# Optimization experiments

Hardware: AMD Instinct MI355X
Metric: run time of the kernel (lower is better)

## Reference

```python
import jax, jax.numpy as jnp
import numpy as np

B, S, H = 2, 2048, 2048
NUM_HEADS, NUM_KV_HEADS, HEAD_DIM = 8, 1, 256
ROPE_THETA = 10000.0
NEG_INF = -1e9


def _rope_tables(seq_len, head_dim, base=ROPE_THETA):
    # cos/sin of shape [seq_len, head_dim], matching GemmaRotaryEmbedding
    inv_freq = 1.0 / (base ** (jnp.arange(0, head_dim, 2, dtype=jnp.float32) / head_dim))
    pos = jnp.arange(seq_len, dtype=jnp.float32)
    freqs = pos[:, None] * inv_freq[None, :]          # [S, D/2]
    emb = jnp.concatenate([freqs, freqs], axis=-1)    # [S, D]
    return jnp.cos(emb), jnp.sin(emb)


def _rotate_half(x):
    d = x.shape[-1] // 2
    return jnp.concatenate([-x[..., d:], x[..., :d]], axis=-1)


def setup_inputs() -> dict:
    key = jax.random.key(0)
    ks = jax.random.split(key, 5)
    hidden_states = jax.random.normal(ks[0], (B, S, H), dtype=jnp.float32)
    # additive causal mask: 0 where allowed, -inf above diagonal
    causal = jnp.tril(jnp.ones((S, S), dtype=bool))
    attention_mask = jnp.where(causal, 0.0, NEG_INF).astype(jnp.float32)[None, None]  # [1,1,S,S]
    sc = 1.0 / np.sqrt(H)
    Wq = jax.random.normal(ks[1], (H, NUM_HEADS * HEAD_DIM), dtype=jnp.float32) * sc
    Wk = jax.random.normal(ks[2], (H, NUM_KV_HEADS * HEAD_DIM), dtype=jnp.float32) * sc
    Wv = jax.random.normal(ks[3], (H, NUM_KV_HEADS * HEAD_DIM), dtype=jnp.float32) * sc
    Wo = jax.random.normal(ks[4], (NUM_HEADS * HEAD_DIM, H), dtype=jnp.float32) * sc
    return {"hidden_states": hidden_states, "attention_mask": attention_mask,
            "Wq": Wq, "Wk": Wk, "Wv": Wv, "Wo": Wo}


def reference(hidden_states, attention_mask, Wq, Wk, Wv, Wo):
    b, s, _ = hidden_states.shape
    g = NUM_HEADS // NUM_KV_HEADS  # query heads per kv head

    q = (hidden_states @ Wq).reshape(b, s, NUM_HEADS, HEAD_DIM).transpose(0, 2, 1, 3)      # [b,h,s,d]
    k = (hidden_states @ Wk).reshape(b, s, NUM_KV_HEADS, HEAD_DIM).transpose(0, 2, 1, 3)   # [b,kh,s,d]
    v = (hidden_states @ Wv).reshape(b, s, NUM_KV_HEADS, HEAD_DIM).transpose(0, 2, 1, 3)   # [b,kh,s,d]

    cos, sin = _rope_tables(s, HEAD_DIM)  # [s,d]
    cos = cos[None, None]                 # [1,1,s,d]
    sin = sin[None, None]
    q = q * cos + _rotate_half(q) * sin
    k = k * cos + _rotate_half(k) * sin

    # GQA attention without materializing repeated K/V: group query heads per kv head
    qg = q.reshape(b, NUM_KV_HEADS, g, s, HEAD_DIM)                       # [b,kh,g,s,d]
    scale = 1.0 / np.sqrt(HEAD_DIM)
    scores = jnp.einsum('bkgsd,bktd->bkgst', qg, k) * scale               # [b,kh,g,s,t]
    scores = scores + attention_mask[:, :, None]                          # broadcast [1,1,1,s,t]
    probs = jax.nn.softmax(scores, axis=-1)
    out = jnp.einsum('bkgst,bktd->bkgsd', probs, v)                       # [b,kh,g,s,d]
    out = out.reshape(b, NUM_HEADS, s, HEAD_DIM).transpose(0, 2, 1, 3).reshape(b, s, NUM_HEADS * HEAD_DIM)
    return out @ Wo
```

## Files before the change

### kernel.cpp

```cpp
#include <hip/hip_runtime.h>

typedef unsigned short u16;
typedef short short8 __attribute__((ext_vector_type(8)));
typedef float f32x4 __attribute__((ext_vector_type(4)));
typedef float f32x16 __attribute__((ext_vector_type(16)));
typedef u16 u16x4 __attribute__((ext_vector_type(4)));

__device__ __forceinline__ u16 f2bf(float f) {
    unsigned int u = __float_as_uint(f);
    u += 0x7fffu + ((u >> 16) & 1u);
    return (u16)(u >> 16);
}
__device__ __forceinline__ float bf2f(u16 s) {
    return __uint_as_float(((unsigned int)s) << 16);
}
__device__ __forceinline__ unsigned pack2(float lo, float hi) {
    return (unsigned)f2bf(lo) | ((unsigned)f2bf(hi) << 16);
}
__device__ __forceinline__ f32x4 mfma16(short8 a, short8 b, f32x4 c) {
    return __builtin_amdgcn_mfma_f32_16x16x32_bf16(a, b, c, 0, 0, 0);
}
__device__ __forceinline__ f32x16 mfma32(short8 a, short8 b, f32x16 c) {
    return __builtin_amdgcn_mfma_f32_32x32x16_bf16(a, b, c, 0, 0, 0);
}
__device__ __forceinline__ void gld16(const void* g, void* l) {
    __builtin_amdgcn_global_load_lds(
        (const __attribute__((address_space(1))) unsigned int*)g,
        (__attribute__((address_space(3))) unsigned int*)l, 16, 0, 0);
}

#define BATCH 2
#define SEQ   2048
#define HID   2048
#define NH    8
#define HD    256
#define MROWS (BATCH * SEQ)

__global__ void k_cvt(const float* __restrict__ src, u16* __restrict__ dst, int n) {
    int i = (blockIdx.x * 256 + threadIdx.x) * 4;
    if (i >= n) return;
    float4 v = *(const float4*)(src + i);
    u16x4 o; o.x = f2bf(v.x); o.y = f2bf(v.y); o.z = f2bf(v.z); o.w = f2bf(v.w);
    *(u16x4*)(dst + i) = o;
}

__global__ __launch_bounds__(256) void k_wt(const float* __restrict__ W,
                                            u16* __restrict__ Wt, int N) {
    __shared__ float tile[64][65];
    const int k0 = blockIdx.y << 6, n0 = blockIdx.x << 6;
    const int tr = threadIdx.x >> 6, tc = threadIdx.x & 63;
#pragma unroll
    for (int i = 0; i < 16; i++)
        tile[i * 4 + tr][tc] = W[(size_t)(k0 + i * 4 + tr) * N + n0 + tc];
    __syncthreads();
#pragma unroll
    for (int i = 0; i < 16; i++) {
        int r = i * 4 + tr;
        Wt[(size_t)(n0 + r) * 2048 + k0 + tc] = f2bf(tile[tc][r]);
    }
}

__global__ __launch_bounds__(256) void k_vt(const u16* __restrict__ KVb, char* __restrict__ VS) {
    __shared__ u16 sT[64][72];
    const int bid = blockIdx.x;
    const int b = bid >> 7, kvt = (bid >> 2) & 31, dc = bid & 3;
    const int tr = threadIdx.x >> 6, tc = threadIdx.x & 63;
#pragma unroll
    for (int i = 0; i < 16; i++) {
        int kv = i * 4 + tr;
        sT[kv][tc] = KVb[((size_t)(b * SEQ + kvt * 64 + kv) << 9) + 256 + (dc << 6) + tc];
    }
    __syncthreads();
    char* obase = VS + ((size_t)b << 20) + (size_t)kvt * 32768;
#pragma unroll
    for (int e = 0; e < 2; e++) {
        int u = threadIdx.x * 2 + e;
        int dl = u >> 3, kvc = u & 7;
        union { u16 h[8]; uint4 q; } pk;
#pragma unroll
        for (int j = 0; j < 8; j++) pk.h[j] = sT[kvc * 8 + j][dl];
        int byte = dl * 512 + ((((dc << 7) + (kvc << 4))) ^ ((dl & 31) << 4));
        *(uint4*)(obase + byte) = pk.q;
    }
}

template<int FUSEQKV>
__global__ __launch_bounds__(256) void k_gemm(const u16* __restrict__ A,
                                              const u16* __restrict__ Bt,
                                              u16* __restrict__ Cq,
                                              u16* __restrict__ Ckv,
                                              float* __restrict__ Cf,
                                              int K, int nbx) {
    const int cpx = gridDim.x >> 3;
    const int t8  = (blockIdx.x & 7) * cpx + (blockIdx.x >> 3);
    const int m0 = (t8 / nbx) << 7;
    const int n0 = (t8 % nbx) << 7;

    const int tid = threadIdx.x, lane = tid & 63, wave = tid >> 6;
    const int g = lane >> 4, c = lane & 15;
    const int wrow = (wave >> 1) << 6, wcol = (wave & 1) << 6;

    __shared__ __align__(16) u16 sA[2][128 * 64];
    __shared__ __align__(16) u16 sB[2][128 * 64];

    const int srow = lane >> 3;
    const int scol = ((lane & 7) ^ srow) << 3;
    const u16* gA = A  + (size_t)(m0 + wave * 32 + srow) * K + scol;
    const u16* gB = Bt + (size_t)(n0 + wave * 32 + srow) * K + scol;
    const int lofs = wave * 32 * 64;

    f32x4 acc[4][4] = {};
    const int nt = K >> 6;

#define STAGE(t, bi)                                                         \
    {                                                                        \
        const int k0s = (t) << 6;                                            \
        _Pragma("unroll")                                                    \
        for (int i = 0; i < 4; i++) {                                        \
            gld16(gA + k0s + (size_t)i * 8 * K, sA[bi] + lofs + i * 8 * 64); \
            gld16(gB + k0s + (size_t)i * 8 * K, sB[bi] + lofs + i * 8 * 64); \
        }                                                                    \
    }

    STAGE(0, 0);
    for (int t = 0; t < nt; t++) {
        const int bi = t & 1;
        __syncthreads();
        if (t + 1 < nt) STAGE(t + 1, bi ^ 1);
#pragma unroll
        for (int ks = 0; ks < 2; ks++) {
            short8 aF[4], bF[4];
#pragma unroll
            for (int tt = 0; tt < 4; tt++) {
                const int ar = wrow + tt * 16 + c;
                const int br = wcol + tt * 16 + c;
                const int coff = ks * 64 + g * 16;
                aF[tt] = *(const short8*)((const char*)sA[bi] + ar * 128 + (coff ^ ((ar & 7) << 4)));
                bF[tt] = *(const short8*)((const char*)sB[bi] + br * 128 + (coff ^ ((br & 7) << 4)));
            }
#pragma unroll
            for (int mt = 0; mt < 4; mt++)
#pragma unroll
                for (int ntc = 0; ntc < 4; ntc++)
                    acc[mt][ntc] = mfma16(aF[mt], bF[ntc], acc[mt][ntc]);
        }
    }
#undef STAGE

#pragma unroll
    for (int mt = 0; mt < 4; mt++)
#pragma unroll
        for (int ntc = 0; ntc < 4; ntc++)
#pragma unroll
            for (int r = 0; r < 4; r++) {
                int row = m0 + wrow + mt * 16 + g * 4 + r;
                int col = n0 + wcol + ntc * 16 + c;
                float v = acc[mt][ntc][r];
                if (FUSEQKV) {
                    if (col < 2048) Cq [(size_t)row * 2048 + col] = f2bf(v);
                    else            Ckv[(size_t)row * 512 + (col - 2048)] = f2bf(v);
                } else {
                    Cf[(size_t)row * 2048 + col] = v;
                }
            }
}

__global__ void k_rope(u16* __restrict__ Qb, const u16* __restrict__ KVb,
                       char* __restrict__ KS) {
    int idx = blockIdx.x * 256 + threadIdx.x;
    const int QP = MROWS * NH * 128;
    if (idx < QP) {
        int row  = idx >> 10;
        int rest = idx & 1023;
        int h = rest >> 7, d = rest & 127;
        u16* base = Qb + (size_t)row * HID + h * HD + d;
        int pos = row & (SEQ - 1);
        float invf = __expf(-(float)d * (9.2103403719761836f / 128.0f));
        float ang = (float)pos * invf;
        float sn, cs; __sincosf(ang, &sn, &cs);
        float x0 = bf2f(base[0]);
        float x1 = bf2f(base[128]);
        base[0]   = f2bf(x0 * cs - x1 * sn);
        base[128] = f2bf(x1 * cs + x0 * sn);
    } else {
        int j = idx - QP;
        int row = j >> 7, d = j & 127;
        const u16* src = KVb + (size_t)row * 512 + d;
        int pos = row & (SEQ - 1);
        float invf = __expf(-(float)d * (9.2103403719761836f / 128.0f));
        float ang = (float)pos * invf;
        float sn, cs; __sincosf(ang, &sn, &cs);
        float x0 = bf2f(src[0]);
        float x1 = bf2f(src[128]);
        int bb = row >> 11, sr = row & 2047;
        char* obase = KS + ((size_t)bb << 20) + (size_t)(sr >> 6) * 32768 + (sr & 63) * 512;
        int xr = ((sr & 31) << 4);
        *(u16*)(obase + (((d << 1))        ^ xr)) = f2bf(x0 * cs - x1 * sn);
        *(u16*)(obase + (((d << 1) + 256)  ^ xr)) = f2bf(x1 * cs + x0 * sn);
    }
}

__global__ __launch_bounds__(512, 2) void k_attn(const u16* __restrict__ Q,
                                                 const char* __restrict__ KS,
                                                 const char* __restrict__ VS,
                                                 u16* __restrict__ Oa) {
    const int tid  = threadIdx.x;
    const int lane = tid & 63;
    const int wave = tid >> 6;
    const int l31  = lane & 31;
    const int hv   = lane >> 5;

    const int bid  = blockIdx.x;
    const int bh   = bid & 15;
    const int a    = bid >> 4;
    const int b = bh >> 3, head = bh & 7;

    const int g   = wave >> 2;
    const int s   = (wave >> 1) & 1;
    const int h   = wave & 1;
    const int qt  = g ? (31 - a) : a;
    const int ntw = g ? (32 - a) : (a + 1);
    const int nt1 = 32 - a;

    __shared__ __align__(16) char smem[133120];
    float* const sML = (float*)(smem + 131072);

    const int qg = qt * 64 + s * 32 + l31;
    short8 qf[16];
    {
        const u16* qptr = Q + (size_t)(b * SEQ + qg) * HID + head * HD + (hv << 3);
#pragma unroll
        for (int ks = 0; ks < 16; ks++)
            qf[ks] = *(const short8*)(qptr + (ks << 4));
    }

    f32x16 o[8] = {};
    float m = -1e30f, l = 0.f;

    const char* kgb = KS + ((size_t)b << 20);
    const char* vgb = VS + ((size_t)b << 20);
    const int kxor = l31 << 4;

#pragma unroll
    for (int i = 0; i < 4; i++) {
        int ch = (i << 3) + wave;
        gld16(kgb + ch * 1024 + lane * 16, smem + ch * 1024);
        gld16(vgb + ch * 1024 + lane * 16, smem + 32768 + ch * 1024);
    }

    for (int t = 0; t < nt1; t++) {
        char* const base = smem + (t & 1) * 65536;
        __syncthreads();
        if (t + 1 < nt1) {
            char* const nb = smem + ((t + 1) & 1) * 65536;
#pragma unroll
            for (int i = 0; i < 4; i++) {
                int ch = (i << 3) + wave;
                gld16(kgb + (size_t)(t + 1) * 32768 + ch * 1024 + lane * 16, nb + ch * 1024);
                gld16(vgb + (size_t)(t + 1) * 32768 + ch * 1024 + lane * 16, nb + 32768 + ch * 1024);
            }
        }
        if (t >= ntw) continue;

        const char* pK = base;
        const char* pV = base + 32768;
        const char* kbase = pK + ((h << 5) + l31) * 512;

        f32x16 sv = {};
        __builtin_amdgcn_s_setprio(1);
#pragma unroll
        for (int ks = 0; ks < 16; ks++) {
            short8 kf = *(const short8*)(kbase + (((ks << 5) + (hv << 4)) ^ kxor));
            sv = mfma32(kf, qf[ks], sv);
        }
        __builtin_amdgcn_s_setprio(0);

        float v[16];
        float mx = -3.0e38f;
        const bool diag = (t == ntw - 1);
#pragma unroll
        for (int r = 0; r < 16; r++) {
            float x = sv[r] * 0.0625f;
            if (diag) {
                int kvg = (t << 6) + (h << 5) + (r & 3) + ((r >> 2) << 3) + (hv << 2);
                if (kvg > qg) x = -3.0e38f;
            }
            v[r] = x;
            mx = fmaxf(mx, x);
        }
        mx = fmaxf(mx, __shfl_xor(mx, 32));
        if (!__all(mx <= m + 8.0f)) {
            float mn = fmaxf(m, mx);
            float sc = __expf(m - mn);
            l *= sc;
#pragma unroll
            for (int r = 0; r < 16; r++) {
                float scr = __shfl(sc, (r & 3) + ((r >> 2) << 3) + (hv << 2));
#pragma unroll
                for (int dt = 0; dt < 8; dt++) o[dt][r] *= scr;
            }
            m = mn;
        }
        float rs = 0.f;
#pragma unroll
        for (int r = 0; r < 16; r++) { v[r] = __expf(v[r] - m); rs += v[r]; }
        rs += __shfl_xor(rs, 32);
        l += rs;

        unsigned wd[8], pw[8];
#pragma unroll
        for (int i = 0; i < 8; i++) wd[i] = pack2(v[2 * i], v[2 * i + 1]);
#pragma unroll
        for (int i = 0; i < 8; i++) pw[i] = (unsigned)__shfl_xor((int)wd[i], 32);

        __builtin_amdgcn_s_setprio(1);
#pragma unroll
        for (int ks2 = 0; ks2 < 2; ks2++) {
            union { unsigned u[4]; short8 s8; } fr;
            const int o4 = ks2 << 2;
            fr.u[0] = hv ? pw[o4 + 2] : wd[o4 + 0];
            fr.u[1] = hv ? pw[o4 + 3] : wd[o4 + 1];
            fr.u[2] = hv ? wd[o4 + 2] : pw[o4 + 0];
            fr.u[3] = hv ? wd[o4 + 3] : pw[o4 + 1];
            const int vcol = (h << 6) + (ks2 << 5) + (hv << 4);
#pragma unroll
            for (int dt = 0; dt < 8; dt++) {
                int row  = ((dt & 1) << 5) + l31;
                int colb = ((dt >> 1) << 7) + vcol;
                short8 vf = *(const short8*)(pV + row * 512 + (colb ^ kxor));
                o[dt] = mfma32(fr.s8, vf, o[dt]);
            }
        }
        __builtin_amdgcn_s_setprio(0);
    }

    __syncthreads();
    if (lane < 32) {
        sML[(wave << 6) + (l31 << 1)]     = m;
        sML[(wave << 6) + (l31 << 1) + 1] = l;
    }
    __syncthreads();
    float m1 = sML[((wave ^ 1) << 6) + (l31 << 1)];
    float l1 = sML[((wave ^ 1) << 6) + (l31 << 1) + 1];
    float M  = fmaxf(m, m1);
    float e0 = __expf(m - M), e1 = __expf(m1 - M);
    float fac = e0 / (l * e0 + l1 * e1);
    float facr[16];
#pragma unroll
    for (int r = 0; r < 16; r++)
        facr[r] = __shfl(fac, (r & 3) + ((r >> 2) << 3) + (hv << 2));
#pragma unroll
    for (int dt = 0; dt < 8; dt++)
#pragma unroll
        for (int r = 0; r < 16; r++) o[dt][r] *= facr[r];

    float* sO = (float*)smem;
    const int p = wave >> 1;
    if (h) {
#pragma unroll
        for (int dt = 0; dt < 8; dt++)
#pragma unroll
            for (int r = 0; r < 16; r++) {
                int q = (r & 3) + ((r >> 2) << 3) + (hv << 2);
                sO[(p << 13) + (q << 8) + (dt << 5) + l31] = o[dt][r];
            }
    }
    __syncthreads();
    if (!h) {
#pragma unroll
        for (int dt = 0; dt < 8; dt++)
#pragma unroll
            for (int r = 0; r < 16; r++) {
                int q = (r & 3) + ((r >> 2) << 3) + (hv << 2);
                float val = o[dt][r] + sO[(p << 13) + (q << 8) + (dt << 5) + l31];
                Oa[(size_t)(b * SEQ + qt * 64 + s * 32 + q) * HID
                   + head * HD + (dt << 5) + l31] = f2bf(val);
            }
    }
}

extern "C" void kernel_launch(void* const* d_in, const int* in_sizes, int n_in,
                              void* d_out, int out_size, void* d_ws, size_t ws_size,
                              hipStream_t stream) {
    const float* hidden = (const float*)d_in[0];
    const float* Wq = (const float*)d_in[2];
    const float* Wk = (const float*)d_in[3];
    const float* Wv = (const float*)d_in[4];
    const float* Wo = (const float*)d_in[5];
    float* out = (float*)d_out;

    char* ws = (char*)d_ws;
    u16* hid_bf = (u16*)(ws);
    u16* Wqkvt  = (u16*)(ws + (16u << 20));
    u16* Wot    = (u16*)(ws + (26u << 20));
    u16* Qb     = (u16*)(ws + (34u << 20));
    u16* KVb    = (u16*)(ws + (50u << 20));
    u16* Ab     = (u16*)(ws + (54u << 20));
    char* KS    = ws;
    char* VS    = ws + (2u << 20);

    k_cvt<<<8192, 256, 0, stream>>>(hidden, hid_bf, MROWS * HID);
    k_wt <<<dim3(32, 32), 256, 0, stream>>>(Wq, Wqkvt, 2048);
    k_wt <<<dim3(4, 32),  256, 0, stream>>>(Wk, Wqkvt + (size_t)2048 * 2048, 256);
    k_wt <<<dim3(4, 32),  256, 0, stream>>>(Wv, Wqkvt + (size_t)2304 * 2048, 256);
    k_wt <<<dim3(32, 32), 256, 0, stream>>>(Wo, Wot, 2048);

    k_gemm<1><<<640, 256, 0, stream>>>(hid_bf, Wqkvt, Qb, KVb, nullptr, 2048, 20);

    k_rope<<<18432, 256, 0, stream>>>(Qb, KVb, KS);
    k_vt  <<<256, 256, 0, stream>>>(KVb, VS);

    k_attn<<<256, 512, 0, stream>>>(Qb, KS, VS, Ab);

    k_gemm<0><<<512, 256, 0, stream>>>(Ab, Wot, nullptr, nullptr, out, 2048, 16);
}
```

Before: 246.2 us.

## Read V fragments directly from global in MFMA layout, halving attention LDS

The V-transpose kernel now writes V pre-arranged in the exact per-lane MFMA B-fragment layout, so the attention kernel reads V fragments straight from global/L2 instead of staging them through LDS. LDS drops from about 130KB to about 66KB, which may allow two workgroups per CU, and the output reduction is split into two passes to fit the smaller buffer. It also splits the QK^T MFMA chain into two independent accumulators and switches bf16 packing to the HIP intrinsic. The risk is global-load latency on V inside the inner loop, since it is no longer prefetched, and the extra barriers in the epilogue.

Measured after the change: 348.8 us. +41.6%, slower.

```diff
diff --git a/kernel.cpp b/kernel.cpp
--- a/kernel.cpp
+++ b/kernel.cpp
@@ -1,4 +1,5 @@
 #include <hip/hip_runtime.h>
+#include <hip/hip_bf16.h>
 
 typedef unsigned short u16;
 typedef short short8 __attribute__((ext_vector_type(8)));
@@ -15,7 +16,9 @@
     return __uint_as_float(((unsigned int)s) << 16);
 }
 __device__ __forceinline__ unsigned pack2(float lo, float hi) {
-    return (unsigned)f2bf(lo) | ((unsigned)f2bf(hi) << 16);
+    union { __hip_bfloat162 h; unsigned u; } cv;
+    cv.h = __float22bfloat162_rn(make_float2(lo, hi));
+    return cv.u;
 }
 __device__ __forceinline__ f32x4 mfma16(short8 a, short8 b, f32x4 c) {
     return __builtin_amdgcn_mfma_f32_16x16x32_bf16(a, b, c, 0, 0, 0);
@@ -75,11 +78,11 @@
 #pragma unroll
     for (int e = 0; e < 2; e++) {
         int u = threadIdx.x * 2 + e;
-        int dl = u >> 3, kvc = u & 7;
+        int kvc = u >> 6, dl = u & 63;
         union { u16 h[8]; uint4 q; } pk;
 #pragma unroll
         for (int j = 0; j < 8; j++) pk.h[j] = sT[kvc * 8 + j][dl];
-        int byte = dl * 512 + ((((dc << 7) + (kvc << 4))) ^ ((dl & 31) << 4));
+        int byte = kvc * 4096 + ((dc << 6) + dl) * 16;
         *(uint4*)(obase + byte) = pk.q;
     }
 }
@@ -222,8 +225,8 @@
     const int ntw = g ? (32 - a) : (a + 1);
     const int nt1 = 32 - a;
 
-    __shared__ __align__(16) char smem[133120];
-    float* const sML = (float*)(smem + 131072);
+    __shared__ __align__(16) char smem[67584];
+    float* const sML = (float*)(smem + 65536);
 
     const int qg = qt * 64 + s * 32 + l31;
     short8 qf[16];
@@ -245,42 +248,42 @@
     for (int i = 0; i < 4; i++) {
         int ch = (i << 3) + wave;
         gld16(kgb + ch * 1024 + lane * 16, smem + ch * 1024);
-        gld16(vgb + ch * 1024 + lane * 16, smem + 32768 + ch * 1024);
     }
 
     for (int t = 0; t < nt1; t++) {
-        char* const base = smem + (t & 1) * 65536;
+        char* const base = smem + (t & 1) * 32768;
         __syncthreads();
         if (t + 1 < nt1) {
-            char* const nb = smem + ((t + 1) & 1) * 65536;
+            char* const nb = smem + ((t + 1) & 1) * 32768;
 #pragma unroll
             for (int i = 0; i < 4; i++) {
                 int ch = (i << 3) + wave;
                 gld16(kgb + (size_t)(t + 1) * 32768 + ch * 1024 + lane * 16, nb + ch * 1024);
-                gld16(vgb + (size_t)(t + 1) * 32768 + ch * 1024 + lane * 16, nb + 32768 + ch * 1024);
             }
         }
         if (t >= ntw) continue;
 
-        const char* pK = base;
-        const char* pV = base + 32768;
-        const char* kbase = pK + ((h << 5) + l31) * 512;
-
-        f32x16 sv = {};
+        const char* kbase = base + ((h << 5) + l31) * 512;
+        const char* vt    = vgb + (size_t)t * 32768;
+
+        f32x16 sv0 = {}, sv1 = {};
         __builtin_amdgcn_s_setprio(1);
 #pragma unroll
-        for (int ks = 0; ks < 16; ks++) {
-            short8 kf = *(const short8*)(kbase + (((ks << 5) + (hv << 4)) ^ kxor));
-            sv = mfma32(kf, qf[ks], sv);
+        for (int ks = 0; ks < 16; ks += 2) {
+            short8 kf0 = *(const short8*)(kbase + (((ks << 5) + (hv << 4)) ^ kxor));
+            short8 kf1 = *(const short8*)(kbase + ((((ks + 1) << 5) + (hv << 4)) ^ kxor));
+            sv0 = mfma32(kf0, qf[ks], sv0);
+            sv1 = mfma32(kf1, qf[ks + 1], sv1);
         }
         __builtin_amdgcn_s_setprio(0);
+        f32x16 svs = sv0 + sv1;
 
         float v[16];
         float mx = -3.0e38f;
         const bool diag = (t == ntw - 1);
 #pragma unroll
         for (int r = 0; r < 16; r++) {
-            float x = sv[r] * 0.0625f;
+            float x = svs[r] * 0.0625f;
             if (diag) {
                 int kvg = (t << 6) + (h << 5) + (r & 3) + ((r >> 2) << 3) + (hv << 2);
                 if (kvg > qg) x = -3.0e38f;
@@ -322,12 +325,10 @@
             fr.u[1] = hv ? pw[o4 + 3] : wd[o4 + 1];
             fr.u[2] = hv ? wd[o4 + 2] : pw[o4 + 0];
             fr.u[3] = hv ? wd[o4 + 3] : pw[o4 + 1];
-            const int vcol = (h << 6) + (ks2 << 5) + (hv << 4);
+            const char* vfb = vt + (((h << 2) + (ks2 << 1) + hv) * 4096) + (l31 << 4);
 #pragma unroll
             for (int dt = 0; dt < 8; dt++) {
-                int row  = ((dt & 1) << 5) + l31;
-                int colb = ((dt >> 1) << 7) + vcol;
-                short8 vf = *(const short8*)(pV + row * 512 + (colb ^ kxor));
+                short8 vf = *(const short8*)(vfb + dt * 512);
                 o[dt] = mfma32(fr.s8, vf, o[dt]);
             }
         }
@@ -356,26 +357,29 @@
 
     float* sO = (float*)smem;
     const int p = wave >> 1;
-    if (h) {
-#pragma unroll
-        for (int dt = 0; dt < 8; dt++)
-#pragma unroll
-            for (int r = 0; r < 16; r++) {
-                int q = (r & 3) + ((r >> 2) << 3) + (hv << 2);
-                sO[(p << 13) + (q << 8) + (dt << 5) + l31] = o[dt][r];
-            }
-    }
-    __syncthreads();
-    if (!h) {
-#pragma unroll
-        for (int dt = 0; dt < 8; dt++)
-#pragma unroll
-            for (int r = 0; r < 16; r++) {
-                int q = (r & 3) + ((r >> 2) << 3) + (hv << 2);
-                float val = o[dt][r] + sO[(p << 13) + (q << 8) + (dt << 5) + l31];
-                Oa[(size_t)(b * SEQ + qt * 64 + s * 32 + q) * HID
-                   + head * HD + (dt << 5) + l31] = f2bf(val);
-            }
+    for (int pass = 0; pass < 2; pass++) {
+        __syncthreads();
+        if ((p >> 1) == pass && h) {
+#pragma unroll
+            for (int dt = 0; dt < 8; dt++)
+#pragma unroll
+                for (int r = 0; r < 16; r++) {
+                    int q = (r & 3) + ((r >> 2) << 3) + (hv << 2);
+                    sO[((p & 1) << 13) + (q << 8) + (dt << 5) + l31] = o[dt][r];
+                }
+        }
+        __syncthreads();
+        if ((p >> 1) == pass && !h) {
+#pragma unroll
+            for (int dt = 0; dt < 8; dt++)
+#pragma unroll
+                for (int r = 0; r < 16; r++) {
+                    int q = (r & 3) + ((r >> 2) << 3) + (hv << 2);
+                    float val = o[dt][r] + sO[((p & 1) << 13) + (q << 8) + (dt << 5) + l31];
+                    Oa[(size_t)(b * SEQ + qt * 64 + s * 32 + q) * HID
+                       + head * HD + (dt << 5) + l31] = f2bf(val);
+                }
+        }
     }
 }
 
```
